# Performance work log

Measured on AMD Instinct MI355X. Metric: run time of the kernel, lower is better.

## Reference

```python
import jax, jax.numpy as jnp
import numpy as np


def setup_inputs() -> dict:
    key = jax.random.key(0)
    k1, k2, k3, k4, k5 = jax.random.split(key, 5)
    b, c, k, h, w = 8, 512, 19, 128, 128
    x = jax.random.normal(k1, (b, c, h, w), dtype=jnp.float32)
    # mask_conv: 1x1 conv ichn->ochn (weight [k, c], bias [k])
    Wm = jax.random.normal(k2, (k, c), dtype=jnp.float32) * (1.0 / np.sqrt(c))
    bm = jax.random.normal(k3, (k,), dtype=jnp.float32) * 0.02
    # filter_conv: grouped 1x1 conv, groups=k -> per-class [c_out, c_in] matmul
    Wf = jax.random.normal(k4, (k, c, c), dtype=jnp.float32) * (1.0 / np.sqrt(c))
    bf = jax.random.normal(k5, (k, c), dtype=jnp.float32) * 0.02
    return {"x": x, "Wm": Wm, "bm": bm, "Wf": Wf, "bf": bf}


def reference(x, Wm, bm, Wf, bf):
    b, c, h, w = x.shape
    k = Wm.shape[0]
    # mask_conv (1x1) + sigmoid -> [b, k, h, w]
    pre_mask = jnp.einsum('bchw,kc->bkhw', x, Wm) + bm[None, :, None, None]
    mask = jax.nn.sigmoid(pre_mask)
    # masked pooling: bmm(mask [b,k,hw], feat [b,hw,c]) / (h*w) -> [b, k, c]
    class_feat = jnp.einsum('bkhw,bchw->bkc', mask, x) / (h * w)
    # grouped 1x1 filter_conv: per class k, [c_out, c_in] GEMM on class_feat
    filters = jnp.einsum('koc,bkc->bko', Wf, class_feat) + bf[None, :, :]  # [b, k, c]
    # per-sample dynamic 1x1 conv (groups=b) == batched GEMM over channels
    pred = jnp.einsum('bkc,bchw->bkhw', filters, x)
    return pred
```

## Files before the change

kernel.cpp:

```cpp
#include <hip/hip_runtime.h>
#include <math.h>

#define BB 8
#define CC 512
#define KK 19
#define HWHW 16384
#define INV_HW (1.0f/16384.0f)

#define SWZ(r) ((((r) ^ ((r) >> 2))) & 7)

typedef __attribute__((ext_vector_type(8))) short bf16x8;
typedef __attribute__((ext_vector_type(4))) short s16x4;
typedef __attribute__((ext_vector_type(4))) float f32x4;

__device__ __forceinline__ short f2bf(float f) {
    unsigned int u = __float_as_uint(f);
    u = (u + 0x7fffu + ((u >> 16) & 1u)) >> 16;
    return (short)u;
}

__global__ __launch_bounds__(256) void k_s1(const float* __restrict__ x,
                                            const float* __restrict__ Wm,
                                            const float* __restrict__ bm,
                                            unsigned short* __restrict__ mask) {
    __shared__ short wm[20 * CC];
    __shared__ short xt[256 * 64];
    const int tid = threadIdx.x;
    const int b = blockIdx.x >> 6;
    const int p0 = (blockIdx.x & 63) << 8;
    const float* xb = x + ((size_t)b * CC) * HWHW + p0;

    for (int u = tid; u < 20 * 128; u += 256) {
        const int k = u >> 7;
        const int c4 = (u & 127) << 2;
        float4 w = {0.f, 0.f, 0.f, 0.f};
        if (k < KK) w = *(const float4*)(Wm + k * CC + c4);
        s16x4 v = { f2bf(w.x), f2bf(w.y), f2bf(w.z), f2bf(w.w) };
        const int chunk = c4 >> 3, half = (c4 >> 2) & 1;
        *(s16x4*)&wm[(k << 9) + ((chunk ^ SWZ(k)) << 3) + (half << 2)] = v;
    }

    const int wv = tid >> 6, ln = tid & 63;
    const int lm = ln & 15, q = ln >> 4;
    const int m1 = (lm < 3) ? (16 + lm) : 19;
    const f32x4 zz = {0.f, 0.f, 0.f, 0.f};
    f32x4 acc[2][4];
#pragma unroll
    for (int i = 0; i < 4; ++i) { acc[0][i] = zz; acc[1][i] = zz; }

    for (int cs = 0; cs < 8; ++cs) {
        __syncthreads();
#pragma unroll
        for (int r = 0; r < 2; ++r) {
            const int u = tid + (r << 8);
            const int cg8 = u >> 6;
            const int p = (u & 63) << 2;
            const float* src = xb + (size_t)((cs << 6) + (cg8 << 3)) * HWHW + p;
            float4 F[8];
#pragma unroll
            for (int i = 0; i < 8; ++i) F[i] = *(const float4*)(src + (size_t)i * HWHW);
            const float* G = (const float*)F;
#pragma unroll
            for (int j = 0; j < 4; ++j) {
                const int pr = p + j;
                bf16x8 v = { f2bf(G[0*4+j]), f2bf(G[1*4+j]), f2bf(G[2*4+j]), f2bf(G[3*4+j]),
                             f2bf(G[4*4+j]), f2bf(G[5*4+j]), f2bf(G[6*4+j]), f2bf(G[7*4+j]) };
                *(bf16x8*)&xt[(pr << 6) + ((cg8 ^ SWZ(pr)) << 3)] = v;
            }
        }
        __syncthreads();
#pragma unroll
        for (int ks = 0; ks < 2; ++ks) {
            const int gch = (cs << 3) + (ks << 2) + q;
            bf16x8 a0 = *(const bf16x8*)&wm[(lm << 9) + ((gch ^ SWZ(lm)) << 3)];
            bf16x8 a1 = *(const bf16x8*)&wm[(m1 << 9) + ((gch ^ SWZ(m1)) << 3)];
            const int lch = (ks << 2) + q;
#pragma unroll
            for (int nt = 0; nt < 4; ++nt) {
                const int pr = (((wv << 2) + nt) << 4) + lm;
                bf16x8 bfr = *(const bf16x8*)&xt[(pr << 6) + ((lch ^ SWZ(pr)) << 3)];
                acc[0][nt] = __builtin_amdgcn_mfma_f32_16x16x32_bf16(a0, bfr, acc[0][nt], 0, 0, 0);
                acc[1][nt] = __builtin_amdgcn_mfma_f32_16x16x32_bf16(a1, bfr, acc[1][nt], 0, 0, 0);
            }
        }
    }

    unsigned short* mb = mask + ((size_t)b * KK) * HWHW + p0;
#pragma unroll
    for (int mt = 0; mt < 2; ++mt)
#pragma unroll
        for (int r = 0; r < 4; ++r) {
            const int k = (mt << 4) + (q << 2) + r;
            if (k < KK) {
                const float bias = bm[k];
#pragma unroll
                for (int nt = 0; nt < 4; ++nt) {
                    const int p = (((wv << 2) + nt) << 4) + lm;
                    const float t = acc[mt][nt][r] + bias;
                    mb[(size_t)k * HWHW + p] = (unsigned short)f2bf(1.0f / (1.0f + __expf(-t)));
                }
            }
        }
}

__global__ __launch_bounds__(256) void k_s2(const float* __restrict__ x,
                                            const unsigned short* __restrict__ mask,
                                            float* __restrict__ cf_part) {
    __shared__ short mt_[20 * 64];
    __shared__ short xtl[512 * 64];
    const int tid = threadIdx.x;
    const int b = blockIdx.x >> 6;
    const int s = blockIdx.x & 63;
    const int wv = tid >> 6, ln = tid & 63;
    const int lm = ln & 15, q = ln >> 4;
    const int m1 = (lm < 3) ? (16 + lm) : 19;
    const float* xb = x + ((size_t)b * CC) * HWHW + (s << 8);
    const unsigned short* mbs = mask + ((size_t)b * KK) * HWHW + (s << 8);

    const f32x4 zz = {0.f, 0.f, 0.f, 0.f};
    f32x4 acc[2][8];
#pragma unroll
    for (int i = 0; i < 8; ++i) { acc[0][i] = zz; acc[1][i] = zz; }

    for (int kp = 0; kp < 4; ++kp) {
        __syncthreads();
        if (tid < 160) {
            const int k = tid >> 3, ch = tid & 7;
            uint4 v = {0u, 0u, 0u, 0u};
            if (k < KK) v = *(const uint4*)(mbs + (size_t)k * HWHW + (kp << 6) + (ch << 3));
            *(uint4*)&mt_[(k << 6) + ((ch ^ SWZ(k)) << 3)] = v;
        }
#pragma unroll
        for (int r = 0; r < 4; ++r) {
            const int u = tid + (r << 8);
            const int cg8 = u >> 4;
            const int pq = u & 15;
            const int p = pq << 2;
            const float* src = xb + (size_t)(cg8 << 3) * HWHW + (kp << 6) + p;
#pragma unroll
            for (int i = 0; i < 8; ++i) {
                float4 f = *(const float4*)(src + (size_t)i * HWHW);
                const int c = (cg8 << 3) + i;
                s16x4 v = { f2bf(f.x), f2bf(f.y), f2bf(f.z), f2bf(f.w) };
                *(s16x4*)&xtl[(c << 6) + (((pq >> 1) ^ SWZ(c)) << 3) + ((pq & 1) << 2)] = v;
            }
        }
        __syncthreads();
#pragma unroll
        for (int ks = 0; ks < 2; ++ks) {
            const int pch = (ks << 2) + q;
            bf16x8 a0 = *(const bf16x8*)&mt_[(lm << 6) + ((pch ^ SWZ(lm)) << 3)];
            bf16x8 a1 = *(const bf16x8*)&mt_[(m1 << 6) + ((pch ^ SWZ(m1)) << 3)];
#pragma unroll
            for (int nt = 0; nt < 8; ++nt) {
                const int c = (((wv << 3) + nt) << 4) + lm;
                bf16x8 bfr = *(const bf16x8*)&xtl[(c << 6) + ((pch ^ SWZ(c)) << 3)];
                acc[0][nt] = __builtin_amdgcn_mfma_f32_16x16x32_bf16(a0, bfr, acc[0][nt], 0, 0, 0);
                acc[1][nt] = __builtin_amdgcn_mfma_f32_16x16x32_bf16(a1, bfr, acc[1][nt], 0, 0, 0);
            }
        }
    }

    float* dst = cf_part + ((size_t)((s << 3) + b) * KK) * CC;
#pragma unroll
    for (int mt = 0; mt < 2; ++mt)
#pragma unroll
        for (int r = 0; r < 4; ++r) {
            const int k = (mt << 4) + (q << 2) + r;
            if (k < KK) {
#pragma unroll
                for (int nt = 0; nt < 8; ++nt) {
                    const int c = (((wv << 3) + nt) << 4) + lm;
                    dst[(size_t)k * CC + c] = acc[mt][nt][r];
                }
            }
        }
}

__global__ __launch_bounds__(256) void k_s2r(const float* __restrict__ part,
                                             float* __restrict__ cf) {
    const int i = blockIdx.x * 256 + threadIdx.x;
    if (i >= BB * KK * CC) return;
    const int b = i / (KK * CC);
    const int rem = i - b * (KK * CC);
    float sum = 0.0f;
#pragma unroll
    for (int s = 0; s < 64; ++s)
        sum += part[((size_t)((s << 3) + b) * KK) * CC + rem];
    cf[i] = sum * INV_HW;
}

__global__ __launch_bounds__(256) void k_filters(const float* __restrict__ Wf,
                                                 const float* __restrict__ bf,
                                                 const float* __restrict__ cf,
                                                 float* __restrict__ fil) {
    const int blk = blockIdx.x;
    const int k = blk >> 7;
    const int o = ((blk & 127) << 2) + (threadIdx.x >> 6);
    const int lane = threadIdx.x & 63;
    const float* wrow = Wf + ((size_t)k * CC + o) * CC;

    float acc[BB];
#pragma unroll
    for (int b = 0; b < BB; ++b) acc[b] = 0.0f;
#pragma unroll
    for (int j = 0; j < CC / 64; ++j) {
        const int c = lane + (j << 6);
        const float wv = wrow[c];
#pragma unroll
        for (int b = 0; b < BB; ++b)
            acc[b] += wv * cf[((size_t)b * KK + k) * CC + c];
    }
#pragma unroll
    for (int b = 0; b < BB; ++b) {
#pragma unroll
        for (int off = 32; off > 0; off >>= 1)
            acc[b] += __shfl_down(acc[b], off, 64);
    }
    if (lane == 0) {
        const float bias = bf[k * CC + o];
#pragma unroll
        for (int b = 0; b < BB; ++b)
            fil[((size_t)b * KK + k) * CC + o] = acc[b] + bias;
    }
}

__global__ __launch_bounds__(256) void k_s4(const float* __restrict__ x,
                                            const float* __restrict__ fil,
                                            float* __restrict__ out) {
    __shared__ short wm[20 * CC];
    __shared__ short xt[256 * 64];
    const int tid = threadIdx.x;
    const int b = blockIdx.x >> 6;
    const int p0 = (blockIdx.x & 63) << 8;
    const float* xb = x + ((size_t)b * CC) * HWHW + p0;
    const float* fb = fil + ((size_t)b * KK) * CC;

    for (int u = tid; u < 20 * 128; u += 256) {
        const int k = u >> 7;
        const int c4 = (u & 127) << 2;
        float4 w = {0.f, 0.f, 0.f, 0.f};
        if (k < KK) w = *(const float4*)(fb + k * CC + c4);
        s16x4 v = { f2bf(w.x), f2bf(w.y), f2bf(w.z), f2bf(w.w) };
        const int chunk = c4 >> 3, half = (c4 >> 2) & 1;
        *(s16x4*)&wm[(k << 9) + ((chunk ^ SWZ(k)) << 3) + (half << 2)] = v;
    }

    const int wv = tid >> 6, ln = tid & 63;
    const int lm = ln & 15, q = ln >> 4;
    const int m1 = (lm < 3) ? (16 + lm) : 19;
    const f32x4 zz = {0.f, 0.f, 0.f, 0.f};
    f32x4 acc[2][4];
#pragma unroll
    for (int i = 0; i < 4; ++i) { acc[0][i] = zz; acc[1][i] = zz; }

    for (int cs = 0; cs < 8; ++cs) {
        __syncthreads();
#pragma unroll
        for (int r = 0; r < 2; ++r) {
            const int u = tid + (r << 8);
            const int cg8 = u >> 6;
            const int p = (u & 63) << 2;
            const float* src = xb + (size_t)((cs << 6) + (cg8 << 3)) * HWHW + p;
            float4 F[8];
#pragma unroll
            for (int i = 0; i < 8; ++i) F[i] = *(const float4*)(src + (size_t)i * HWHW);
            const float* G = (const float*)F;
#pragma unroll
            for (int j = 0; j < 4; ++j) {
                const int pr = p + j;
                bf16x8 v = { f2bf(G[0*4+j]), f2bf(G[1*4+j]), f2bf(G[2*4+j]), f2bf(G[3*4+j]),
                             f2bf(G[4*4+j]), f2bf(G[5*4+j]), f2bf(G[6*4+j]), f2bf(G[7*4+j]) };
                *(bf16x8*)&xt[(pr << 6) + ((cg8 ^ SWZ(pr)) << 3)] = v;
            }
        }
        __syncthreads();
#pragma unroll
        for (int ks = 0; ks < 2; ++ks) {
            const int gch = (cs << 3) + (ks << 2) + q;
            bf16x8 a0 = *(const bf16x8*)&wm[(lm << 9) + ((gch ^ SWZ(lm)) << 3)];
            bf16x8 a1 = *(const bf16x8*)&wm[(m1 << 9) + ((gch ^ SWZ(m1)) << 3)];
            const int lch = (ks << 2) + q;
#pragma unroll
            for (int nt = 0; nt < 4; ++nt) {
                const int pr = (((wv << 2) + nt) << 4) + lm;
                bf16x8 bfr = *(const bf16x8*)&xt[(pr << 6) + ((lch ^ SWZ(pr)) << 3)];
                acc[0][nt] = __builtin_amdgcn_mfma_f32_16x16x32_bf16(a0, bfr, acc[0][nt], 0, 0, 0);
                acc[1][nt] = __builtin_amdgcn_mfma_f32_16x16x32_bf16(a1, bfr, acc[1][nt], 0, 0, 0);
            }
        }
    }

    float* ob = out + ((size_t)b * KK) * HWHW + p0;
#pragma unroll
    for (int mt = 0; mt < 2; ++mt)
#pragma unroll
        for (int r = 0; r < 4; ++r) {
            const int k = (mt << 4) + (q << 2) + r;
            if (k < KK) {
#pragma unroll
                for (int nt = 0; nt < 4; ++nt) {
                    const int p = (((wv << 2) + nt) << 4) + lm;
                    ob[(size_t)k * HWHW + p] = acc[mt][nt][r];
                }
            }
        }
}

extern "C" void kernel_launch(void* const* d_in, const int* in_sizes, int n_in,
                              void* d_out, int out_size, void* d_ws, size_t ws_size,
                              hipStream_t stream) {
    const float* x  = (const float*)d_in[0];
    const float* Wm = (const float*)d_in[1];
    const float* bm = (const float*)d_in[2];
    const float* Wf = (const float*)d_in[3];
    const float* bf = (const float*)d_in[4];
    float* out = (float*)d_out;

    unsigned short* mask = (unsigned short*)d_ws;
    float* cf_part = (float*)((char*)d_ws + (size_t)BB * KK * HWHW * 2);
    float* cf  = cf_part + (size_t)64 * BB * KK * CC;
    float* fil = cf + (size_t)BB * KK * CC;

    k_s1<<<512, 256, 0, stream>>>(x, Wm, bm, mask);
    k_s2<<<512, 256, 0, stream>>>(x, mask, cf_part);
    k_s2r<<<(BB * KK * CC + 255) / 256, 256, 0, stream>>>(cf_part, cf);
    k_filters<<<KK * 128, 256, 0, stream>>>(Wf, bf, cf, fil);
    k_s4<<<512, 256, 0, stream>>>(x, fil, out);
}
```

Before: 499.8 us.

## Fuse mask and pooling kernels; load x fragments directly from global

Merges the mask GEMM and masked-pooling GEMM into one kernel, so the sigmoid mask stays in shared memory and the bf16 mask round trip through global memory goes away. Both this kernel and the final prediction kernel drop the shared-memory staging of transposed x tiles. Each lane now gathers its MFMA B-fragment straight from global memory: scalar strided loads across channels in the first and last GEMMs, and float4 loads in the pooling GEMM. This removes barriers and LDS traffic, but the channel-strided scalar loads may coalesce poorly and raise global memory transactions. Padded LDS rows replace the XOR swizzle.

```diff
diff --git a/kernel.cpp b/kernel.cpp
--- a/kernel.cpp
+++ b/kernel.cpp
@@ -7,8 +7,6 @@
 #define HWHW 16384
 #define INV_HW (1.0f/16384.0f)
 
-#define SWZ(r) ((((r) ^ ((r) >> 2))) & 7)
-
 typedef __attribute__((ext_vector_type(8))) short bf16x8;
 typedef __attribute__((ext_vector_type(4))) short s16x4;
 typedef __attribute__((ext_vector_type(4))) float f32x4;
@@ -19,16 +17,17 @@
     return (short)u;
 }
 
-__global__ __launch_bounds__(256) void k_s1(const float* __restrict__ x,
-                                            const float* __restrict__ Wm,
-                                            const float* __restrict__ bm,
-                                            unsigned short* __restrict__ mask) {
-    __shared__ short wm[20 * CC];
-    __shared__ short xt[256 * 64];
+__global__ __launch_bounds__(256) void k_s12(const float* __restrict__ x,
+                                             const float* __restrict__ Wm,
+                                             const float* __restrict__ bm,
+                                             float* __restrict__ cf_part) {
+    __shared__ short wm[20][520];
+    __shared__ short ml[20][264];
     const int tid = threadIdx.x;
     const int b = blockIdx.x >> 6;
-    const int p0 = (blockIdx.x & 63) << 8;
-    const float* xb = x + ((size_t)b * CC) * HWHW + p0;
+    const int s = blockIdx.x & 63;
+    const int p0 = s << 8;
+    const float* xb = x + (size_t)b * CC * HWHW;
 
     for (int u = tid; u < 20 * 128; u += 256) {
         const int k = u >> 7;
@@ -36,56 +35,38 @@
         float4 w = {0.f, 0.f, 0.f, 0.f};
         if (k < KK) w = *(const float4*)(Wm + k * CC + c4);
         s16x4 v = { f2bf(w.x), f2bf(w.y), f2bf(w.z), f2bf(w.w) };
-        const int chunk = c4 >> 3, half = (c4 >> 2) & 1;
-        *(s16x4*)&wm[(k << 9) + ((chunk ^ SWZ(k)) << 3) + (half << 2)] = v;
-    }
+        *(s16x4*)&wm[k][c4] = v;
+    }
+    if (tid < 66) { s16x4 z = {0, 0, 0, 0}; *(s16x4*)&ml[19][tid << 2] = z; }
+    __syncthreads();
 
     const int wv = tid >> 6, ln = tid & 63;
     const int lm = ln & 15, q = ln >> 4;
     const int m1 = (lm < 3) ? (16 + lm) : 19;
+    const int pw = p0 + (wv << 6);
+
     const f32x4 zz = {0.f, 0.f, 0.f, 0.f};
-    f32x4 acc[2][4];
-#pragma unroll
-    for (int i = 0; i < 4; ++i) { acc[0][i] = zz; acc[1][i] = zz; }
-
-    for (int cs = 0; cs < 8; ++cs) {
-        __syncthreads();
-#pragma unroll
-        for (int r = 0; r < 2; ++r) {
-            const int u = tid + (r << 8);
-            const int cg8 = u >> 6;
-            const int p = (u & 63) << 2;
-            const float* src = xb + (size_t)((cs << 6) + (cg8 << 3)) * HWHW + p;
-            float4 F[8];
-#pragma unroll
-            for (int i = 0; i < 8; ++i) F[i] = *(const float4*)(src + (size_t)i * HWHW);
-            const float* G = (const float*)F;
-#pragma unroll
-            for (int j = 0; j < 4; ++j) {
-                const int pr = p + j;
-                bf16x8 v = { f2bf(G[0*4+j]), f2bf(G[1*4+j]), f2bf(G[2*4+j]), f2bf(G[3*4+j]),
-                             f2bf(G[4*4+j]), f2bf(G[5*4+j]), f2bf(G[6*4+j]), f2bf(G[7*4+j]) };
-                *(bf16x8*)&xt[(pr << 6) + ((cg8 ^ SWZ(pr)) << 3)] = v;
-            }
-        }
-        __syncthreads();
-#pragma unroll
-        for (int ks = 0; ks < 2; ++ks) {
-            const int gch = (cs << 3) + (ks << 2) + q;
-            bf16x8 a0 = *(const bf16x8*)&wm[(lm << 9) + ((gch ^ SWZ(lm)) << 3)];
-            bf16x8 a1 = *(const bf16x8*)&wm[(m1 << 9) + ((gch ^ SWZ(m1)) << 3)];
-            const int lch = (ks << 2) + q;
-#pragma unroll
-            for (int nt = 0; nt < 4; ++nt) {
-                const int pr = (((wv << 2) + nt) << 4) + lm;
-                bf16x8 bfr = *(const bf16x8*)&xt[(pr << 6) + ((lch ^ SWZ(pr)) << 3)];
-                acc[0][nt] = __builtin_amdgcn_mfma_f32_16x16x32_bf16(a0, bfr, acc[0][nt], 0, 0, 0);
-                acc[1][nt] = __builtin_amdgcn_mfma_f32_16x16x32_bf16(a1, bfr, acc[1][nt], 0, 0, 0);
-            }
-        }
-    }
-
-    unsigned short* mb = mask + ((size_t)b * KK) * HWHW + p0;
+    f32x4 accA[2][4];
+#pragma unroll
+    for (int i = 0; i < 4; ++i) { accA[0][i] = zz; accA[1][i] = zz; }
+
+    for (int cs = 0; cs < 16; ++cs) {
+        const int cbase = (cs << 5) + (q << 3);
+        bf16x8 a0 = *(const bf16x8*)&wm[lm][cbase];
+        bf16x8 a1 = *(const bf16x8*)&wm[m1][cbase];
+        const float* col = xb + (size_t)cbase * HWHW;
+#pragma unroll
+        for (int nt = 0; nt < 4; ++nt) {
+            const int p = pw + (nt << 4) + lm;
+            bf16x8 bv;
+#pragma unroll
+            for (int j = 0; j < 8; ++j)
+                bv[j] = f2bf(col[(size_t)j * HWHW + p]);
+            accA[0][nt] = __builtin_amdgcn_mfma_f32_16x16x32_bf16(a0, bv, accA[0][nt], 0, 0, 0);
+            accA[1][nt] = __builtin_amdgcn_mfma_f32_16x16x32_bf16(a1, bv, accA[1][nt], 0, 0, 0);
+        }
+    }
+
 #pragma unroll
     for (int mt = 0; mt < 2; ++mt)
 #pragma unroll
@@ -95,69 +76,32 @@
                 const float bias = bm[k];
 #pragma unroll
                 for (int nt = 0; nt < 4; ++nt) {
-                    const int p = (((wv << 2) + nt) << 4) + lm;
-                    const float t = acc[mt][nt][r] + bias;
-                    mb[(size_t)k * HWHW + p] = (unsigned short)f2bf(1.0f / (1.0f + __expf(-t)));
+                    const float t = accA[mt][nt][r] + bias;
+                    ml[k][(wv << 6) + (nt << 4) + lm] = f2bf(1.0f / (1.0f + __expf(-t)));
                 }
             }
         }
-}
-
-__global__ __launch_bounds__(256) void k_s2(const float* __restrict__ x,
-                                            const unsigned short* __restrict__ mask,
-                                            float* __restrict__ cf_part) {
-    __shared__ short mt_[20 * 64];
-    __shared__ short xtl[512 * 64];
-    const int tid = threadIdx.x;
-    const int b = blockIdx.x >> 6;
-    const int s = blockIdx.x & 63;
-    const int wv = tid >> 6, ln = tid & 63;
-    const int lm = ln & 15, q = ln >> 4;
-    const int m1 = (lm < 3) ? (16 + lm) : 19;
-    const float* xb = x + ((size_t)b * CC) * HWHW + (s << 8);
-    const unsigned short* mbs = mask + ((size_t)b * KK) * HWHW + (s << 8);
-
-    const f32x4 zz = {0.f, 0.f, 0.f, 0.f};
-    f32x4 acc[2][8];
-#pragma unroll
-    for (int i = 0; i < 8; ++i) { acc[0][i] = zz; acc[1][i] = zz; }
-
-    for (int kp = 0; kp < 4; ++kp) {
-        __syncthreads();
-        if (tid < 160) {
-            const int k = tid >> 3, ch = tid & 7;
-            uint4 v = {0u, 0u, 0u, 0u};
-            if (k < KK) v = *(const uint4*)(mbs + (size_t)k * HWHW + (kp << 6) + (ch << 3));
-            *(uint4*)&mt_[(k << 6) + ((ch ^ SWZ(k)) << 3)] = v;
-        }
-#pragma unroll
-        for (int r = 0; r < 4; ++r) {
-            const int u = tid + (r << 8);
-            const int cg8 = u >> 4;
-            const int pq = u & 15;
-            const int p = pq << 2;
-            const float* src = xb + (size_t)(cg8 << 3) * HWHW + (kp << 6) + p;
-#pragma unroll
-            for (int i = 0; i < 8; ++i) {
-                float4 f = *(const float4*)(src + (size_t)i * HWHW);
-                const int c = (cg8 << 3) + i;
-                s16x4 v = { f2bf(f.x), f2bf(f.y), f2bf(f.z), f2bf(f.w) };
-                *(s16x4*)&xtl[(c << 6) + (((pq >> 1) ^ SWZ(c)) << 3) + ((pq & 1) << 2)] = v;
-            }
-        }
-        __syncthreads();
-#pragma unroll
-        for (int ks = 0; ks < 2; ++ks) {
-            const int pch = (ks << 2) + q;
-            bf16x8 a0 = *(const bf16x8*)&mt_[(lm << 6) + ((pch ^ SWZ(lm)) << 3)];
-            bf16x8 a1 = *(const bf16x8*)&mt_[(m1 << 6) + ((pch ^ SWZ(m1)) << 3)];
-#pragma unroll
-            for (int nt = 0; nt < 8; ++nt) {
-                const int c = (((wv << 3) + nt) << 4) + lm;
-                bf16x8 bfr = *(const bf16x8*)&xtl[(c << 6) + ((pch ^ SWZ(c)) << 3)];
-                acc[0][nt] = __builtin_amdgcn_mfma_f32_16x16x32_bf16(a0, bfr, acc[0][nt], 0, 0, 0);
-                acc[1][nt] = __builtin_amdgcn_mfma_f32_16x16x32_bf16(a1, bfr, acc[1][nt], 0, 0, 0);
-            }
+    __syncthreads();
+
+    f32x4 acc2[2][8];
+#pragma unroll
+    for (int i = 0; i < 8; ++i) { acc2[0][i] = zz; acc2[1][i] = zz; }
+
+    const float* xp = xb + p0;
+    for (int ks = 0; ks < 8; ++ks) {
+        const int pb = (ks << 5) + (q << 3);
+        bf16x8 a0 = *(const bf16x8*)&ml[lm][pb];
+        bf16x8 a1 = *(const bf16x8*)&ml[m1][pb];
+#pragma unroll
+        for (int cnt = 0; cnt < 8; ++cnt) {
+            const int c = (wv << 7) + (cnt << 4) + lm;
+            const float* src = xp + (size_t)c * HWHW + pb;
+            float4 f0 = *(const float4*)(src);
+            float4 f1 = *(const float4*)(src + 4);
+            bf16x8 bv = { f2bf(f0.x), f2bf(f0.y), f2bf(f0.z), f2bf(f0.w),
+                          f2bf(f1.x), f2bf(f1.y), f2bf(f1.z), f2bf(f1.w) };
+            acc2[0][cnt] = __builtin_amdgcn_mfma_f32_16x16x32_bf16(a0, bv, acc2[0][cnt], 0, 0, 0);
+            acc2[1][cnt] = __builtin_amdgcn_mfma_f32_16x16x32_bf16(a1, bv, acc2[1][cnt], 0, 0, 0);
         }
     }
 
@@ -169,9 +113,9 @@
             const int k = (mt << 4) + (q << 2) + r;
             if (k < KK) {
 #pragma unroll
-                for (int nt = 0; nt < 8; ++nt) {
-                    const int c = (((wv << 3) + nt) << 4) + lm;
-                    dst[(size_t)k * CC + c] = acc[mt][nt][r];
+                for (int cnt = 0; cnt < 8; ++cnt) {
+                    const int c = (wv << 7) + (cnt << 4) + lm;
+                    dst[(size_t)k * CC + c] = acc2[mt][cnt][r];
                 }
             }
         }
@@ -228,13 +172,12 @@
 __global__ __launch_bounds__(256) void k_s4(const float* __restrict__ x,
                                             const float* __restrict__ fil,
                                             float* __restrict__ out) {
-    __shared__ short wm[20 * CC];
-    __shared__ short xt[256 * 64];
+    __shared__ short wm[20][520];
     const int tid = threadIdx.x;
     const int b = blockIdx.x >> 6;
     const int p0 = (blockIdx.x & 63) << 8;
-    const float* xb = x + ((size_t)b * CC) * HWHW + p0;
-    const float* fb = fil + ((size_t)b * KK) * CC;
+    const float* xb = x + (size_t)b * CC * HWHW;
+    const float* fb = fil + (size_t)b * KK * CC;
 
     for (int u = tid; u < 20 * 128; u += 256) {
         const int k = u >> 7;
@@ -242,56 +185,38 @@
         float4 w = {0.f, 0.f, 0.f, 0.f};
         if (k < KK) w = *(const float4*)(fb + k * CC + c4);
         s16x4 v = { f2bf(w.x), f2bf(w.y), f2bf(w.z), f2bf(w.w) };
-        const int chunk = c4 >> 3, half = (c4 >> 2) & 1;
-        *(s16x4*)&wm[(k << 9) + ((chunk ^ SWZ(k)) << 3) + (half << 2)] = v;
-    }
+        *(s16x4*)&wm[k][c4] = v;
+    }
+    __syncthreads();
 
     const int wv = tid >> 6, ln = tid & 63;
     const int lm = ln & 15, q = ln >> 4;
     const int m1 = (lm < 3) ? (16 + lm) : 19;
+    const int pw = p0 + (wv << 6);
+
     const f32x4 zz = {0.f, 0.f, 0.f, 0.f};
     f32x4 acc[2][4];
 #pragma unroll
     for (int i = 0; i < 4; ++i) { acc[0][i] = zz; acc[1][i] = zz; }
 
-    for (int cs = 0; cs < 8; ++cs) {
-        __syncthreads();
-#pragma unroll
-        for (int r = 0; r < 2; ++r) {
-            const int u = tid + (r << 8);
-            const int cg8 = u >> 6;
-            const int p = (u & 63) << 2;
-            const float* src = xb + (size_t)((cs << 6) + (cg8 << 3)) * HWHW + p;
-            float4 F[8];
-#pragma unroll
-            for (int i = 0; i < 8; ++i) F[i] = *(const float4*)(src + (size_t)i * HWHW);
-            const float* G = (const float*)F;
-#pragma unroll
-            for (int j = 0; j < 4; ++j) {
-                const int pr = p + j;
-                bf16x8 v = { f2bf(G[0*4+j]), f2bf(G[1*4+j]), f2bf(G[2*4+j]), f2bf(G[3*4+j]),
-                             f2bf(G[4*4+j]), f2bf(G[5*4+j]), f2bf(G[6*4+j]), f2bf(G[7*4+j]) };
-                *(bf16x8*)&xt[(pr << 6) + ((cg8 ^ SWZ(pr)) << 3)] = v;
-            }
-        }
-        __syncthreads();
-#pragma unroll
-        for (int ks = 0; ks < 2; ++ks) {
-            const int gch = (cs << 3) + (ks << 2) + q;
-            bf16x8 a0 = *(const bf16x8*)&wm[(lm << 9) + ((gch ^ SWZ(lm)) << 3)];
-            bf16x8 a1 = *(const bf16x8*)&wm[(m1 << 9) + ((gch ^ SWZ(m1)) << 3)];
-            const int lch = (ks << 2) + q;
-#pragma unroll
-            for (int nt = 0; nt < 4; ++nt) {
-                const int pr = (((wv << 2) + nt) << 4) + lm;
-                bf16x8 bfr = *(const bf16x8*)&xt[(pr << 6) + ((lch ^ SWZ(pr)) << 3)];
-                acc[0][nt] = __builtin_amdgcn_mfma_f32_16x16x32_bf16(a0, bfr, acc[0][nt], 0, 0, 0);
-                acc[1][nt] = __builtin_amdgcn_mfma_f32_16x16x32_bf16(a1, bfr, acc[1][nt], 0, 0, 0);
-            }
-        }
-    }
-
-    float* ob = out + ((size_t)b * KK) * HWHW + p0;
+    for (int cs = 0; cs < 16; ++cs) {
+        const int cbase = (cs << 5) + (q << 3);
+        bf16x8 a0 = *(const bf16x8*)&wm[lm][cbase];
+        bf16x8 a1 = *(const bf16x8*)&wm[m1][cbase];
+        const float* col = xb + (size_t)cbase * HWHW;
+#pragma unroll
+        for (int nt = 0; nt < 4; ++nt) {
+            const int p = pw + (nt << 4) + lm;
+            bf16x8 bv;
+#pragma unroll
+            for (int j = 0; j < 8; ++j)
+                bv[j] = f2bf(col[(size_t)j * HWHW + p]);
+            acc[0][nt] = __builtin_amdgcn_mfma_f32_16x16x32_bf16(a0, bv, acc[0][nt], 0, 0, 0);
+            acc[1][nt] = __builtin_amdgcn_mfma_f32_16x16x32_bf16(a1, bv, acc[1][nt], 0, 0, 0);
+        }
+    }
+
+    float* ob = out + (size_t)b * KK * HWHW;
 #pragma unroll
     for (int mt = 0; mt < 2; ++mt)
 #pragma unroll
@@ -300,7 +225,7 @@
             if (k < KK) {
 #pragma unroll
                 for (int nt = 0; nt < 4; ++nt) {
-                    const int p = (((wv << 2) + nt) << 4) + lm;
+                    const int p = pw + (nt << 4) + lm;
                     ob[(size_t)k * HWHW + p] = acc[mt][nt][r];
                 }
             }
@@ -317,13 +242,11 @@
     const float* bf = (const float*)d_in[4];
     float* out = (float*)d_out;
 
-    unsigned short* mask = (unsigned short*)d_ws;
-    float* cf_part = (float*)((char*)d_ws + (size_t)BB * KK * HWHW * 2);
+    float* cf_part = (float*)d_ws;
     float* cf  = cf_part + (size_t)64 * BB * KK * CC;
     float* fil = cf + (size_t)BB * KK * CC;
 
-    k_s1<<<512, 256, 0, stream>>>(x, Wm, bm, mask);
-    k_s2<<<512, 256, 0, stream>>>(x, mask, cf_part);
+    k_s12<<<512, 256, 0, stream>>>(x, Wm, bm, cf_part);
     k_s2r<<<(BB * KK * CC + 255) / 256, 256, 0, stream>>>(cf_part, cf);
     k_filters<<<KK * 128, 256, 0, stream>>>(Wf, bf, cf, fil);
     k_s4<<<512, 256, 0, stream>>>(x, fil, out);
```

New measurement: 505.5 us. Within noise of the previous version (+1.1%).
